# Kernel optimization log

Measured on AMD Instinct MI355X. Metric: run time of the kernel, lower is better.

## Reference

```python
import jax, jax.numpy as jnp
import numpy as np
import math


def ste_round(x):
    # round with straight-through gradient (identity in bwd)
    return x + jax.lax.stop_gradient(jnp.round(x) - x)


def ste_floor(x):
    return x + jax.lax.stop_gradient(jnp.floor(x) - x)


def _conv(x, w, b):
    # 5x5 stride-2 conv, padding=2 (kernel_size//2), NCHW/OIHW
    y = jax.lax.conv_general_dilated(
        x, w, window_strides=(2, 2), padding=[(2, 2), (2, 2)],
        dimension_numbers=('NCHW', 'OIHW', 'NCHW'))
    return y + b[None, :, None, None]


def _split_conv(x, w, b_int, mul, split=4):
    # 4 redundant sub-convolutions with floor-STE quantized integer weights/biases
    wq = ste_round(w)  # wSTE: round-to-int with STE
    out = 0.0
    for i in range(split):
        out = out + _conv(x, ste_floor((wq + i) / split), ste_floor((b_int + i) / split))
    return out * mul[None, :, None, None]


def _forward(x, w0, b0, w1, b1, w2, b2, w3, b3, mul0, mul1, mul2, mul3,
             relu0, relu1, relu2, md0, md1, md2, md3, ga_left):
    Bits = 8; clp_k = 8; in_scale = 8; scl_k = 3
    relus = [relu0, relu1, relu2]
    clp = [round((2 ** Bits - 1) / r * 2 ** (16 + clp_k)) for r in relus]
    scl = [math.floor((r + 2 ** (scl_k - 1)) / 2 ** scl_k) for r in relus]

    # quantize input to uint8 range
    x = jnp.clip(ste_round(x * 2 ** in_scale), 0, 255)

    # ---- layer 0 ----
    x = _split_conv(x, w0, ste_round(b0 * 2 ** in_scale), mul0)
    x = ste_floor((x + 2.0 ** (md0 - 1 + in_scale - clp_k)) / 2.0 ** (md0 + in_scale - clp_k))
    x = jnp.clip(x, 0, clp[0])
    x = ste_floor((ste_round(x * scl[0]) + 2.0 ** (15 + clp_k - scl_k)) / 2.0 ** (16 + clp_k - scl_k))

    # ---- layers 1, 2 ----
    for w_, b_, mul_, md_, idx in ((w1, b1, mul1, md1, 1), (w2, b2, mul2, md2, 2)):
        x = _split_conv(x, w_, ste_round(b_), mul_)
        x = ste_floor((x + 2.0 ** (md_ - 1 - clp_k)) / 2.0 ** (md_ - clp_k))
        x = jnp.clip(x, 0, clp[idx])
        x = ste_floor((ste_round(x * scl[idx]) + 2.0 ** (15 + clp_k - scl_k)) / 2.0 ** (16 + clp_k - scl_k))

    # ---- layer 3 (latent) ----
    x = _split_conv(x, w3, ste_round(b3), mul3)
    x = ste_floor((x + 2.0 ** (md3 - 1 - ga_left)) / 2.0 ** (md3 - ga_left))
    return x


def setup_inputs():
    key = jax.random.key(0)
    ks = jax.random.split(key, 16)
    N, M = 192, 320
    d = {}
    d['x'] = jax.random.uniform(ks[0], (4, 3, 512, 512), dtype=jnp.float32)
    # float weights whose round() gives small ints (integerized LIC weights)
    d['w0'] = jax.random.normal(ks[1], (N, 3, 5, 5), dtype=jnp.float32) * 3.0
    d['b0'] = jax.random.normal(ks[2], (N,), dtype=jnp.float32)
    d['w1'] = jax.random.normal(ks[3], (N, N, 5, 5), dtype=jnp.float32) * 3.0
    d['b1'] = jax.random.normal(ks[4], (N,), dtype=jnp.float32) * 16.0
    d['w2'] = jax.random.normal(ks[5], (N, N, 5, 5), dtype=jnp.float32) * 3.0
    d['b2'] = jax.random.normal(ks[6], (N,), dtype=jnp.float32) * 16.0
    d['w3'] = jax.random.normal(ks[7], (M, N, 5, 5), dtype=jnp.float32) * 3.0
    d['b3'] = jax.random.normal(ks[8], (M,), dtype=jnp.float32) * 16.0
    # per-channel integer-valued fixed-point multipliers
    d['mul0'] = jax.random.randint(ks[9], (N,), 1, 64).astype(jnp.float32)
    d['mul1'] = jax.random.randint(ks[10], (N,), 1, 64).astype(jnp.float32)
    d['mul2'] = jax.random.randint(ks[11], (N,), 1, 64).astype(jnp.float32)
    d['mul3'] = jax.random.randint(ks[12], (M,), 1, 64).astype(jnp.float32)
    d['relu0'] = 65536; d['relu1'] = 65536; d['relu2'] = 65536
    d['md0'] = 7; d['md1'] = 15; d['md2'] = 15; d['md3'] = 10
    d['ga_left'] = 4
    return d


def reference(x, w0, b0, w1, b1, w2, b2, w3, b3, mul0, mul1, mul2, mul3,
              relu0, relu1, relu2, md0, md1, md2, md3, ga_left):
    return _forward(x, w0, b0, w1, b1, w2, b2, w3, b3, mul0, mul1, mul2, mul3,
                    relu0, relu1, relu2, md0, md1, md2, md3, ga_left)
```

## Files before the change

### kernel.cpp

```cpp
#include <hip/hip_runtime.h>
#include <hip/hip_bf16.h>

typedef int i32x4 __attribute__((ext_vector_type(4)));
typedef unsigned int u32;
typedef unsigned long long u64;
typedef long long ll;

__device__ __forceinline__ void load_lds16(const void* g, void* l) {
  __builtin_amdgcn_global_load_lds(
      (const __attribute__((address_space(1))) u32*)g,
      (__attribute__((address_space(3))) u32*)l, 16, 0, 0);
}

__global__ __launch_bounds__(256) void prep_all(
    const float* __restrict__ w0, const float* __restrict__ w1,
    const float* __restrict__ w2, const float* __restrict__ w3,
    signed char* __restrict__ w0q, signed char* __restrict__ w1p,
    signed char* __restrict__ w2p, signed char* __restrict__ w3p,
    signed char* __restrict__ zbuf,
    int* __restrict__ totw0, int* __restrict__ totw1,
    int* __restrict__ totw2, int* __restrict__ totw3)
{
  __shared__ signed char ldsw[8 * 4800];
  const int blk = blockIdx.x;
  const int tid = threadIdx.x;

  if (blk < 88) {
    const float* wsrc; signed char* wdst; int* tot; int MF, sub;
    if (blk < 24)      { wsrc = w1; wdst = w1p; tot = totw1; MF = 12; sub = blk; }
    else if (blk < 48) { wsrc = w2; wdst = w2p; tot = totw2; MF = 12; sub = blk - 24; }
    else               { wsrc = w3; wdst = w3p; tot = totw3; MF = 20; sub = blk - 48; }
    const int mf = sub >> 1, half = sub & 1, colbase = half * 8;
    const int ocb = mf * 16 + colbase;
    for (int o = 0; o < 8; o++) {
      const float* src = wsrc + (size_t)(ocb + o) * 4800;
      int s = 0;
      for (int j = tid; j < 4800; j += 256) {
        int v = (int)rintf(src[j]);
        ldsw[o * 4800 + j] = (signed char)v;
        s += v;
      }
      atomicAdd(&tot[ocb + o], s);
    }
    __syncthreads();
    for (int u = tid; u < 9600; u += 256) {
      int eu = u & 3, colL = (u >> 2) & 7, q = (u >> 5) & 3, t = u >> 7;
      int tap = t / 3, ch = t - 3 * tap;
      int ci0 = ch * 64 + q * 16 + eu * 4;
      const signed char* sp = ldsw + colL * 4800 + tap;
      u32 wv = 0;
      #pragma unroll
      for (int bb = 0; bb < 4; bb++)
        wv |= ((u32)(unsigned char)sp[(ci0 + bb) * 25]) << (8 * bb);
      *(u32*)(wdst + ((size_t)t * MF + mf) * 1024 +
              (q * 16 + colbase + colL) * 16 + eu * 4) = wv;
    }
  } else {
    if (tid < 128) ((u64*)zbuf)[tid] = 0x8080808080808080ULL;
    for (int i = tid; i < 24576; i += 256) {
      int e = i & 15, colA = (i >> 4) & 15, q = (i >> 8) & 3, t = i >> 10;
      int mf = t % 12, ch = t / 12;
      signed char v = 0;
      if (e < 15 && (ch == 0 || q == 0)) {
        int ky = (ch == 0) ? q : 4;
        int ci = e / 5, kx = e - ci * 5;
        v = (signed char)(int)rintf(
            w0[((mf * 16 + colA) * 3 + ci) * 25 + ky * 5 + kx]);
      }
      w0q[i] = v;
    }
    for (int oc = tid; oc < 192; oc += 256) {
      const float* p = w0 + (size_t)oc * 75;
      int s = 0;
      #pragma unroll 5
      for (int j = 0; j < 75; j++) s += (int)rintf(p[j]);
      totw0[oc] = s;
    }
  }
}

__global__ __launch_bounds__(192, 3) void conv0F(
    const float* __restrict__ x, const signed char* __restrict__ wq,
    const float* __restrict__ bias, const float* __restrict__ mulv,
    const int* __restrict__ totw,
    const int* __restrict__ reluP, const int* __restrict__ mdP,
    unsigned char* __restrict__ outA)
{
  __shared__ signed char ilds[3][5][132];

  const int tid = threadIdx.x;
  const int lane = tid & 63;
  const int col = lane & 15;
  const int quad = lane >> 4;
  const int w = tid >> 6;
  const int blk = blockIdx.x;
  const int oxblk = blk & 3;
  const int oy = (blk >> 2) & 255;
  const int b = blk >> 10;
  const int oxbase = oxblk * 64;

  i32x4 afr[2][4];
  #pragma unroll
  for (int ch = 0; ch < 2; ch++)
    #pragma unroll
    for (int i = 0; i < 4; i++)
      afr[ch][i] = *(const i32x4*)(wq + ch * 12288 + (w * 4 + i) * 1024 + lane * 16);

  const float* xb = x + (size_t)b * 3 * 512 * 512;
  for (int i = tid; i < 990; i += 192) {
    int j = i % 66; int t = i / 66; int r = t % 5; int ci = t / 5;
    int iy = 2 * oy - 2 + r;
    int ix = 2 * oxbase - 2 + 2 * j;
    int v0 = -128, v1 = -128;
    if ((unsigned)iy < 512u) {
      const float* row = xb + ((size_t)ci * 512 + iy) * 512;
      if ((unsigned)ix < 512u) {
        float xv = rintf(row[ix] * 256.0f);
        v0 = (int)fminf(fmaxf(xv, 0.0f), 255.0f) - 128;
      }
      if ((unsigned)(ix + 1) < 512u) {
        float xv = rintf(row[ix + 1] * 256.0f);
        v1 = (int)fminf(fmaxf(xv, 0.0f), 255.0f) - 128;
      }
    }
    *(unsigned short*)&ilds[ci][r][2 * j] =
        (unsigned short)((v0 & 0xFF) | ((v1 & 0xFF) << 8));
  }
  __syncthreads();

  i32x4 acc[4][4];
  #pragma unroll
  for (int fm = 0; fm < 4; fm++)
    #pragma unroll
    for (int fn = 0; fn < 4; fn++) acc[fm][fn] = (i32x4){0, 0, 0, 0};

  #pragma unroll
  for (int ch = 0; ch < 2; ch++) {
    const int row = (ch == 0) ? quad : 4;
    i32x4 bfr[4];
    #pragma unroll
    for (int fn = 0; fn < 4; fn++) {
      const int xb2 = 2 * (fn * 16 + col);
      const int o8 = (xb2 & 3) * 8;
      const int ab = xb2 & ~3;
      u64 w0_, w1_, w2_;
      {
        const u32* p0 = (const u32*)&ilds[0][row][ab];
        const u32* p1 = (const u32*)&ilds[1][row][ab];
        const u32* p2 = (const u32*)&ilds[2][row][ab];
        w0_ = (u64)p0[0] | ((u64)p0[1] << 32);
        w1_ = (u64)p1[0] | ((u64)p1[1] << 32);
        w2_ = (u64)p2[0] | ((u64)p2[1] << 32);
      }
      u32 a0 = (u32)(w0_ >> o8);
      u32 a1 = ((u32)(w0_ >> (o8 + 32)) & 0xFFu) | (((u32)(w1_ >> o8)) << 8);
      u32 a2 = ((u32)(w1_ >> (o8 + 24)) & 0xFFFFu) | (((u32)(w2_ >> o8)) << 16);
      u32 a3 = (u32)(w2_ >> (o8 + 16));
      bfr[fn] = (i32x4){(int)a0, (int)a1, (int)a2, (int)a3};
    }
    #pragma unroll
    for (int fm = 0; fm < 4; fm++)
      #pragma unroll
      for (int fn = 0; fn < 4; fn++)
        acc[fm][fn] = __builtin_amdgcn_mfma_i32_16x16x64_i8(
            afr[ch][fm], bfr[fn], acc[fm][fn], 0, 0, 0);
  }

  const size_t pix0 = ((size_t)(b * 256 + oy)) * 256 + oxbase;
  const int rl = reluP[0];
  const int sh = mdP[0];
  const ll clpv_ll = llrint(255.0 / (double)rl * 16777216.0);
  const int clpv = clpv_ll > 0x7FFFFFFFLL ? 0x7FFFFFFF : (int)clpv_ll;
  const int sclv = (int)((rl + 4) >> 3);
  const int rnd = 1 << (sh - 1);
  #pragma unroll
  for (int fm = 0; fm < 4; fm++) {
    const int oc0 = w * 64 + fm * 16 + quad * 4;
    int bim[4], mu32[4];
    #pragma unroll
    for (int r = 0; r < 4; r++) {
      int bi = (int)llrintf(bias[oc0 + r] * 256.0f) + 128 * totw[oc0 + r];
      mu32[r] = (int)llrintf(mulv[oc0 + r]);
      bim[r] = bi * mu32[r];
    }
    #pragma unroll
    for (int fn = 0; fn < 4; fn++) {
      const size_t pix = pix0 + fn * 16 + col;
      u32 wd = 0;
      #pragma unroll
      for (int r = 0; r < 4; r++) {
        int vi = acc[fm][fn][r] * mu32[r] + bim[r];
        int y = (vi + rnd) >> sh;
        y = y < 0 ? 0 : (y > clpv ? clpv : y);
        y = (y * sclv + (1 << 20)) >> 21;
        wd |= (((u32)y ^ 0x80u) & 0xFFu) << (8 * r);
      }
      *(u32*)(outA + pix * 192 + oc0) = wd;
    }
  }
}

template <int COUT, int HIN, int WIN, int HOUT, int WOUT, int WV,
          int KSPLIT, bool DIRECT, int NH>
__global__ __launch_bounds__(WV * 64, 2) void convS(
    const signed char* __restrict__ act, const signed char* __restrict__ wp,
    const float* __restrict__ bias, const float* __restrict__ mulv,
    const int* __restrict__ totw,
    const int* __restrict__ reluP, const int* __restrict__ mdP,
    const signed char* __restrict__ zbuf,
    unsigned char* __restrict__ outA, int* __restrict__ outP)
{
  constexpr int CIN = 192;
  constexpr int PASSES = 4;
  constexpr int MF = COUT / 16;
  constexpr int OCW = COUT / WV;
  constexpr int FM = OCW / 16;
  constexpr int SAe = MF * 1024;
  constexpr int TX = WOUT / (16 * NH);
  constexpr int TYB = HOUT / 4;
  constexpr int TPP = 25 / KSPLIT;
  constexpr int NSTEP = TPP * 3;
  constexpr int NB = PASSES * NH;
  constexpr int BUFB = NB * 1024;
  constexpr int SMAX = (NB + WV - 1) / WV;
  constexpr int PSZ = 4 * HOUT * WOUT * COUT;
  static_assert(WV * OCW == COUT, "M covers COUT");
  static_assert(NSTEP >= 4, "pipeline depth");

  __shared__ __align__(16) char smem[4 * BUFB];

  const int tid = threadIdx.x;
  const int lane = tid & 63;
  const int col = lane & 15;
  const int quad = lane >> 4;
  const int w = tid >> 6;
  const int part = blockIdx.y;

  int bx = blockIdx.x;
  const int tx = bx % TX; bx /= TX;
  const int ty = bx % TYB;
  const int b = bx / TYB;
  const int ox0 = tx * 16 * NH;
  const int oy0 = ty * 4;
  const int tap0 = part * TPP;

  const signed char* bp[SMAX];
  int mjx[SMAX], mjy[SMAX];
  #pragma unroll
  for (int k = 0; k < SMAX; k++) {
    const int j = w + k * WV;
    if (j < NB) {
      const int p = j / NH, h = j % NH;
      const int oxv = ox0 + h * 16 + col;
      const int oyv = oy0 + p;
      bp[k] = act + ((size_t)b * HIN * WIN + (size_t)(2 * oyv) * WIN + 2 * oxv) * CIN
              + quad * 16;
      int mx = 0, my = 0;
      #pragma unroll
      for (int kk = 0; kk < 5; kk++) {
        if ((unsigned)(2 * oxv + kk - 2) < (unsigned)WIN) mx |= 1 << kk;
        if ((unsigned)(2 * oyv + kk - 2) < (unsigned)HIN) my |= 1 << kk;
      }
      mjx[k] = mx; mjy[k] = my;
    }
  }
  int kyS = tap0 / 5, kxS = tap0 - 5 * kyS, chS = 0;
  auto stage = [&](int sel) {
    const int offB = ((kyS - 2) * WIN + (kxS - 2)) * CIN + chS * 64;
    #pragma unroll
    for (int k = 0; k < SMAX; k++) {
      const int j = w + k * WV;
      if (j < NB) {
        bool v = ((mjx[k] >> kxS) & 1) && ((mjy[k] >> kyS) & 1);
        const signed char* g = v ? (bp[k] + offB) : (zbuf + quad * 16);
        load_lds16(g, smem + sel * BUFB + j * 1024);
      }
    }
    chS++;
    if (chS == 3) { chS = 0; kxS++; if (kxS == 5) { kxS = 0; kyS++; } }
  };

  i32x4 acc[FM][NB];
  #pragma unroll
  for (int fm = 0; fm < FM; fm++)
    #pragma unroll
    for (int j = 0; j < NB; j++) acc[fm][j] = (i32x4){0, 0, 0, 0};

  const signed char* aptr = wp + (size_t)(tap0 * 3) * SAe + w * FM * 1024 + lane * 16;
  i32x4 aA[FM], aB[FM];
  #pragma unroll
  for (int i = 0; i < FM; i++) aA[i] = *(const i32x4*)(aptr + i * 1024);

  auto comp = [&](int base, i32x4 (&a)[FM]) {
    const char* pB = smem + base + lane * 16;
    i32x4 bfr[NB];
    #pragma unroll
    for (int i = 0; i < NB; i++)
      bfr[i] = *(const i32x4*)(pB + i * 1024);
    #pragma unroll
    for (int fm = 0; fm < FM; fm++)
      #pragma unroll
      for (int j = 0; j < NB; j++)
        acc[fm][j] = __builtin_amdgcn_mfma_i32_16x16x64_i8(
            a[fm], bfr[j], acc[fm][j], 0, 0, 0);
  };

  stage(0); stage(1); stage(2);
  if constexpr (SMAX == 2) asm volatile("s_waitcnt vmcnt(4)" ::: "memory");
  else                     asm volatile("s_waitcnt vmcnt(2)" ::: "memory");
  asm volatile("s_barrier" ::: "memory");

  int sl = 0;
  #pragma unroll 1
  for (; sl + 1 < NSTEP; sl += 2) {
    aptr += SAe;
    #pragma unroll
    for (int i = 0; i < FM; i++) aB[i] = *(const i32x4*)(aptr + i * 1024);
    if (sl + 3 < NSTEP) stage((sl + 3) & 3);
    comp((sl & 3) * BUFB, aA);
    asm volatile("s_barrier" ::: "memory");
    if (sl + 2 < NSTEP) {
      aptr += SAe;
      #pragma unroll
      for (int i = 0; i < FM; i++) aA[i] = *(const i32x4*)(aptr + i * 1024);
    }
    if (sl + 4 < NSTEP) stage((sl + 4) & 3);
    comp(((sl + 1) & 3) * BUFB, aB);
    if (sl + 2 < NSTEP) asm volatile("s_barrier" ::: "memory");
  }
  if (sl < NSTEP) {
    comp((sl & 3) * BUFB, aA);
  }

  if constexpr (DIRECT) {
    const int rl = reluP[0];
    const int sh = mdP[0] - 8;
    const ll clpv = llrint(255.0 / (double)rl * 16777216.0);
    const ll sclv = (ll)((rl + 4) >> 3);
    #pragma unroll
    for (int fm = 0; fm < FM; fm++) {
      const int oc0 = w * OCW + fm * 16 + quad * 4;
      ll bi[4], mu[4];
      #pragma unroll
      for (int r = 0; r < 4; r++) {
        bi[r] = llrintf(bias[oc0 + r]) + 128LL * totw[oc0 + r];
        mu[r] = llrintf(mulv[oc0 + r]);
      }
      #pragma unroll
      for (int j = 0; j < NB; j++) {
        const int p = j / NH, h = j % NH;
        const int oyv = oy0 + p;
        const int oxv = ox0 + h * 16 + col;
        u32 wd = 0;
        #pragma unroll
        for (int r = 0; r < 4; r++) {
          ll vi = ((ll)acc[fm][j][r] + bi[r]) * mu[r];
          ll y = (vi + (1LL << (sh - 1))) >> sh;
          y = y < 0 ? 0LL : (y > clpv ? clpv : y);
          y = (y * sclv + (1LL << 20)) >> 21;
          wd |= (((u32)y ^ 0x80u) & 0xFFu) << (8 * r);
        }
        *(u32*)(outA + ((size_t)((b * HOUT + oyv) * WOUT + oxv)) * COUT + oc0) = wd;
      }
    }
  } else {
    int* pout = outP + (size_t)part * PSZ;
    #pragma unroll
    for (int fm = 0; fm < FM; fm++) {
      const int oc0 = w * OCW + fm * 16 + quad * 4;
      #pragma unroll
      for (int j = 0; j < NB; j++) {
        const int p = j / NH, h = j % NH;
        const int oyv = oy0 + p;
        const int oxv = ox0 + h * 16 + col;
        *(i32x4*)(pout + ((size_t)((b * HOUT + oyv) * WOUT + oxv)) * COUT + oc0) =
            acc[fm][j];
      }
    }
  }
}

__global__ __launch_bounds__(256) void reduce2(
    const int* __restrict__ partP, const float* __restrict__ bias,
    const float* __restrict__ mulv, const int* __restrict__ totw,
    const int* __restrict__ reluP, const int* __restrict__ mdP,
    unsigned char* __restrict__ outA)
{
  const int gid = blockIdx.x * 256 + threadIdx.x;
  const int PSZ4 = 4 * 64 * 64 * 192 / 4;
  const int4* pp = (const int4*)partP;
  int4 sv = pp[gid];
  #pragma unroll
  for (int p = 1; p < 5; p++) {
    int4 v = pp[(size_t)p * PSZ4 + gid];
    sv.x += v.x; sv.y += v.y; sv.z += v.z; sv.w += v.w;
  }
  int sa[4] = {sv.x, sv.y, sv.z, sv.w};
  const int oc0 = (gid * 4) % 192;
  const int rl = reluP[0];
  const int sh = mdP[0] - 8;
  const ll clpv = llrint(255.0 / (double)rl * 16777216.0);
  const ll sclv = (ll)((rl + 4) >> 3);
  u32 wd = 0;
  #pragma unroll
  for (int r = 0; r < 4; r++) {
    ll bi = llrintf(bias[oc0 + r]) + 128LL * totw[oc0 + r];
    ll mu = llrintf(mulv[oc0 + r]);
    ll vi = ((ll)sa[r] + bi) * mu;
    ll y = (vi + (1LL << (sh - 1))) >> sh;
    y = y < 0 ? 0LL : (y > clpv ? clpv : y);
    y = (y * sclv + (1LL << 20)) >> 21;
    wd |= (((u32)y ^ 0x80u) & 0xFFu) << (8 * r);
  }
  ((u32*)outA)[gid] = wd;
}

__global__ __launch_bounds__(256) void reduce3(
    const int* __restrict__ partP, const float* __restrict__ b3,
    const float* __restrict__ mul3, const int* __restrict__ totw3,
    const int* __restrict__ mdP, const int* __restrict__ gaP,
    float* __restrict__ outF)
{
  const int gid = blockIdx.x * 256 + threadIdx.x;
  int t = gid;
  const int ox = t & 31; t >>= 5;
  const int oy = t & 31; t >>= 5;
  const int oc = t % 320;
  const int b  = t / 320;
  const int PSZ = 4 * 32 * 32 * 320;
  const size_t src = ((size_t)((b * 32 + oy) * 32 + ox)) * 320 + oc;
  ll s = 0;
  #pragma unroll
  for (int p = 0; p < 5; p++) s += partP[(size_t)p * PSZ + src];
  const int sh = mdP[0] - gaP[0];
  const ll bi = llrintf(b3[oc]) + 128LL * totw3[oc];
  const ll mu = llrintf(mul3[oc]);
  const ll y = ((s + bi) * mu + (1LL << (sh - 1))) >> sh;
  outF[gid] = (float)y;
}

extern "C" void kernel_launch(void* const* d_in, const int* in_sizes, int n_in,
                              void* d_out, int out_size, void* d_ws, size_t ws_size,
                              hipStream_t stream)
{
  const float* x    = (const float*)d_in[0];
  const float* w0   = (const float*)d_in[1];
  const float* b0   = (const float*)d_in[2];
  const float* w1   = (const float*)d_in[3];
  const float* b1   = (const float*)d_in[4];
  const float* w2   = (const float*)d_in[5];
  const float* b2   = (const float*)d_in[6];
  const float* w3   = (const float*)d_in[7];
  const float* b3   = (const float*)d_in[8];
  const float* mul0 = (const float*)d_in[9];
  const float* mul1 = (const float*)d_in[10];
  const float* mul2 = (const float*)d_in[11];
  const float* mul3 = (const float*)d_in[12];
  const int* relu0  = (const int*)d_in[13];
  const int* relu1  = (const int*)d_in[14];
  const int* relu2  = (const int*)d_in[15];
  const int* md0    = (const int*)d_in[16];
  const int* md1    = (const int*)d_in[17];
  const int* md2    = (const int*)d_in[18];
  const int* md3    = (const int*)d_in[19];
  const int* ga     = (const int*)d_in[20];

  char* ws = (char*)d_ws;
  size_t off = 0;
  signed char* zbuf = (signed char*)(ws + off); off += 1024;
  signed char* w0q  = (signed char*)(ws + off); off += 24576;
  signed char* w1p  = (signed char*)(ws + off); off += 921600;
  signed char* w2p  = (signed char*)(ws + off); off += 921600;
  signed char* w3p  = (signed char*)(ws + off); off += 1536000;
  int*         totw1= (int*)        (ws + off); off += 192 * 4;
  int*         totw2= (int*)        (ws + off); off += 192 * 4;
  int*         totw3= (int*)        (ws + off); off += 320 * 4;
  int*         totw0= (int*)        (ws + off); off += 192 * 4;
  unsigned char* act1 = (unsigned char*)(ws + off); off += (size_t)4 * 256 * 256 * 192;
  unsigned char* act2 = (unsigned char*)(ws + off); off += (size_t)4 * 128 * 128 * 192;
  unsigned char* act3 = (unsigned char*)(ws + off); off += (size_t)4 * 64 * 64 * 192;
  int*         partl  = (int*)(ws + off); off += (size_t)5 * 4 * 64 * 64 * 192 * 4;
  (void)ws_size; (void)in_sizes; (void)n_in; (void)out_size;

  hipMemsetAsync(totw1, 0, (192 + 192 + 320 + 192) * 4, stream);
  prep_all<<<89, 256, 0, stream>>>(w0, w1, w2, w3, w0q, w1p, w2p, w3p,
                                   zbuf, totw0, totw1, totw2, totw3);
  conv0F<<<4096, 192, 0, stream>>>(x, w0q, b0, mul0, totw0, relu0, md0, act1);
  convS<192, 256, 256, 128, 128, 4, 1, true, 2><<<dim3(512, 1), 256, 0, stream>>>(
      (const signed char*)act1, w1p, b1, mul1, totw1, relu1, md1, zbuf, act2, nullptr);
  convS<192, 128, 128, 64, 64, 4, 5, false, 2><<<dim3(128, 5), 256, 0, stream>>>(
      (const signed char*)act2, w2p, b2, mul2, totw2, relu2, md2, zbuf, nullptr, partl);
  reduce2<<<3072, 256, 0, stream>>>(partl, b2, mul2, totw2, relu2, md2, act3);
  convS<320, 64, 64, 32, 32, 5, 5, false, 1><<<dim3(64, 5), 320, 0, stream>>>(
      (const signed char*)act3, w3p, b3, mul3, totw3, nullptr, md3, zbuf, nullptr, partl);
  reduce3<<<5120, 256, 0, stream>>>(partl, b3, mul3, totw3, md3, ga, (float*)d_out);
}
```

Before: 332.5 us.

## Deepen conv staging to a six-slot LDS ring with two MFMA steps per barrier

```diff
diff --git a/kernel.cpp b/kernel.cpp
--- a/kernel.cpp
+++ b/kernel.cpp
@@ -222,12 +222,15 @@
   constexpr int NSTEP = TPP * 3;
   constexpr int NB = PASSES * NH;
   constexpr int BUFB = NB * 1024;
+  constexpr int RING = 6;
   constexpr int SMAX = (NB + WV - 1) / WV;
+  constexpr int NSUP2 = NSTEP / 4;
+  constexpr int VC = 2 * (NB >= WV ? NB / WV : 1);
   constexpr int PSZ = 4 * HOUT * WOUT * COUT;
   static_assert(WV * OCW == COUT, "M covers COUT");
-  static_assert(NSTEP >= 4, "pipeline depth");
-
-  __shared__ __align__(16) char smem[4 * BUFB];
+  static_assert(NSTEP % 4 == 3, "tail structure assumes NSTEP = 4k+3");
+
+  __shared__ __align__(16) char smem[RING * BUFB];
 
   const int tid = threadIdx.x;
   const int lane = tid & 63;
@@ -265,7 +268,8 @@
     }
   }
   int kyS = tap0 / 5, kxS = tap0 - 5 * kyS, chS = 0;
-  auto stage = [&](int sel) {
+  int ssl = 0;
+  auto stage = [&]() {
     const int offB = ((kyS - 2) * WIN + (kxS - 2)) * CIN + chS * 64;
     #pragma unroll
     for (int k = 0; k < SMAX; k++) {
@@ -273,11 +277,12 @@
       if (j < NB) {
         bool v = ((mjx[k] >> kxS) & 1) && ((mjy[k] >> kyS) & 1);
         const signed char* g = v ? (bp[k] + offB) : (zbuf + quad * 16);
-        load_lds16(g, smem + sel * BUFB + j * 1024);
+        load_lds16(g, smem + ssl * BUFB + j * 1024);
       }
     }
     chS++;
     if (chS == 3) { chS = 0; kxS++; if (kxS == 5) { kxS = 0; kyS++; } }
+    ssl = (ssl + 1 == RING) ? 0 : ssl + 1;
   };
 
   i32x4 acc[FM][NB];
@@ -286,13 +291,16 @@
     #pragma unroll
     for (int j = 0; j < NB; j++) acc[fm][j] = (i32x4){0, 0, 0, 0};
 
-  const signed char* aptr = wp + (size_t)(tap0 * 3) * SAe + w * FM * 1024 + lane * 16;
-  i32x4 aA[FM], aB[FM];
-  #pragma unroll
-  for (int i = 0; i < FM; i++) aA[i] = *(const i32x4*)(aptr + i * 1024);
-
-  auto comp = [&](int base, i32x4 (&a)[FM]) {
-    const char* pB = smem + base + lane * 16;
+  auto loadA = [&](int u, i32x4 (&dst)[FM]) {
+    const signed char* p = wp + (size_t)(tap0 * 3 + u) * SAe + w * FM * 1024 + lane * 16;
+    #pragma unroll
+    for (int i = 0; i < FM; i++) dst[i] = *(const i32x4*)(p + i * 1024);
+  };
+
+  int rb = 0;
+  auto cslot = [&]() { int t = rb; rb = (rb + 1 == RING) ? 0 : rb + 1; return t; };
+  auto comp = [&](int slot, i32x4 (&a)[FM]) {
+    const char* pB = smem + slot * BUFB + lane * 16;
     i32x4 bfr[NB];
     #pragma unroll
     for (int i = 0; i < NB; i++)
@@ -305,32 +313,30 @@
             a[fm], bfr[j], acc[fm][j], 0, 0, 0);
   };
 
-  stage(0); stage(1); stage(2);
-  if constexpr (SMAX == 2) asm volatile("s_waitcnt vmcnt(4)" ::: "memory");
-  else                     asm volatile("s_waitcnt vmcnt(2)" ::: "memory");
+  i32x4 a0[FM], a1[FM], a2[FM], a3[FM];
+  loadA(0, a0); loadA(1, a1);
+  stage(); stage(); stage(); stage();
+  if constexpr (VC == 4) asm volatile("s_waitcnt vmcnt(4)" ::: "memory");
+  else                   asm volatile("s_waitcnt vmcnt(2)" ::: "memory");
   asm volatile("s_barrier" ::: "memory");
 
-  int sl = 0;
   #pragma unroll 1
-  for (; sl + 1 < NSTEP; sl += 2) {
-    aptr += SAe;
-    #pragma unroll
-    for (int i = 0; i < FM; i++) aB[i] = *(const i32x4*)(aptr + i * 1024);
-    if (sl + 3 < NSTEP) stage((sl + 3) & 3);
-    comp((sl & 3) * BUFB, aA);
+  for (int i2 = 0; i2 < NSUP2; ++i2) {
+    const int u0 = 4 * i2;
+    loadA(u0 + 2, a2); loadA(u0 + 3, a3);
+    stage(); stage();
+    comp(cslot(), a0); comp(cslot(), a1);
     asm volatile("s_barrier" ::: "memory");
-    if (sl + 2 < NSTEP) {
-      aptr += SAe;
-      #pragma unroll
-      for (int i = 0; i < FM; i++) aA[i] = *(const i32x4*)(aptr + i * 1024);
-    }
-    if (sl + 4 < NSTEP) stage((sl + 4) & 3);
-    comp(((sl + 1) & 3) * BUFB, aB);
-    if (sl + 2 < NSTEP) asm volatile("s_barrier" ::: "memory");
-  }
-  if (sl < NSTEP) {
-    comp((sl & 3) * BUFB, aA);
-  }
+    loadA(u0 + 4, a0); loadA(u0 + 5, a1);
+    stage();
+    if (u0 + 7 < NSTEP) stage();
+    comp(cslot(), a2); comp(cslot(), a3);
+    asm volatile("s_barrier" ::: "memory");
+  }
+  loadA(NSTEP - 1, a2);
+  comp(cslot(), a0); comp(cslot(), a1);
+  asm volatile("s_barrier" ::: "memory");
+  comp(cslot(), a2);
 
   if constexpr (DIRECT) {
     const int rl = reluP[0];
```

Measured after the change: 343.7 us. 1.03x slower.

## Split layers 2 and 3 convolutions by input-channel chunk instead of tap range

Applied to the files above, without the earlier changes.

```diff
diff --git a/kernel.cpp b/kernel.cpp
--- a/kernel.cpp
+++ b/kernel.cpp
@@ -112,16 +112,12 @@
     int iy = 2 * oy - 2 + r;
     int ix = 2 * oxbase - 2 + 2 * j;
     int v0 = -128, v1 = -128;
-    if ((unsigned)iy < 512u) {
-      const float* row = xb + ((size_t)ci * 512 + iy) * 512;
-      if ((unsigned)ix < 512u) {
-        float xv = rintf(row[ix] * 256.0f);
-        v0 = (int)fminf(fmaxf(xv, 0.0f), 255.0f) - 128;
-      }
-      if ((unsigned)(ix + 1) < 512u) {
-        float xv = rintf(row[ix + 1] * 256.0f);
-        v1 = (int)fminf(fmaxf(xv, 0.0f), 255.0f) - 128;
-      }
+    if ((unsigned)iy < 512u && (unsigned)ix < 512u) {
+      const float2 xv = *(const float2*)(xb + ((size_t)ci * 512 + iy) * 512 + ix);
+      float a0 = rintf(xv.x * 256.0f);
+      float a1 = rintf(xv.y * 256.0f);
+      v0 = (int)fminf(fmaxf(a0, 0.0f), 255.0f) - 128;
+      v1 = (int)fminf(fmaxf(a1, 0.0f), 255.0f) - 128;
     }
     *(unsigned short*)&ilds[ci][r][2 * j] =
         (unsigned short)((v0 & 0xFF) | ((v1 & 0xFF) << 8));
@@ -201,7 +197,7 @@
 }
 
 template <int COUT, int HIN, int WIN, int HOUT, int WOUT, int WV,
-          int KSPLIT, bool DIRECT, int NH>
+          int NPART, bool CHS, bool DIRECT, int NH>
 __global__ __launch_bounds__(WV * 64, 2) void convS(
     const signed char* __restrict__ act, const signed char* __restrict__ wp,
     const float* __restrict__ bias, const float* __restrict__ mulv,
@@ -216,10 +212,11 @@
   constexpr int OCW = COUT / WV;
   constexpr int FM = OCW / 16;
   constexpr int SAe = MF * 1024;
+  constexpr int ASTRIDE = CHS ? 3 * SAe : SAe;
   constexpr int TX = WOUT / (16 * NH);
   constexpr int TYB = HOUT / 4;
-  constexpr int TPP = 25 / KSPLIT;
-  constexpr int NSTEP = TPP * 3;
+  constexpr int TPP = CHS ? 25 : 25 / NPART;
+  constexpr int NSTEP = CHS ? 25 : TPP * 3;
   constexpr int NB = PASSES * NH;
   constexpr int BUFB = NB * 1024;
   constexpr int SMAX = (NB + WV - 1) / WV;
@@ -242,7 +239,7 @@
   const int b = bx / TYB;
   const int ox0 = tx * 16 * NH;
   const int oy0 = ty * 4;
-  const int tap0 = part * TPP;
+  const int tap0 = CHS ? 0 : part * TPP;
 
   const signed char* bp[SMAX];
   int mjx[SMAX], mjy[SMAX];
@@ -264,7 +261,8 @@
       mjx[k] = mx; mjy[k] = my;
     }
   }
-  int kyS = tap0 / 5, kxS = tap0 - 5 * kyS, chS = 0;
+  int kyS = tap0 / 5, kxS = tap0 - 5 * kyS;
+  int chS = CHS ? part : 0;
   auto stage = [&](int sel) {
     const int offB = ((kyS - 2) * WIN + (kxS - 2)) * CIN + chS * 64;
     #pragma unroll
@@ -276,8 +274,12 @@
         load_lds16(g, smem + sel * BUFB + j * 1024);
       }
     }
-    chS++;
-    if (chS == 3) { chS = 0; kxS++; if (kxS == 5) { kxS = 0; kyS++; } }
+    if constexpr (CHS) {
+      kxS++; if (kxS == 5) { kxS = 0; kyS++; }
+    } else {
+      chS++;
+      if (chS == 3) { chS = 0; kxS++; if (kxS == 5) { kxS = 0; kyS++; } }
+    }
   };
 
   i32x4 acc[FM][NB];
@@ -286,7 +288,8 @@
     #pragma unroll
     for (int j = 0; j < NB; j++) acc[fm][j] = (i32x4){0, 0, 0, 0};
 
-  const signed char* aptr = wp + (size_t)(tap0 * 3) * SAe + w * FM * 1024 + lane * 16;
+  const signed char* aptr = wp + (size_t)(CHS ? part : tap0 * 3) * SAe
+                            + w * FM * 1024 + lane * 16;
   i32x4 aA[FM], aB[FM];
   #pragma unroll
   for (int i = 0; i < FM; i++) aA[i] = *(const i32x4*)(aptr + i * 1024);
@@ -313,14 +316,14 @@
   int sl = 0;
   #pragma unroll 1
   for (; sl + 1 < NSTEP; sl += 2) {
-    aptr += SAe;
+    aptr += ASTRIDE;
     #pragma unroll
     for (int i = 0; i < FM; i++) aB[i] = *(const i32x4*)(aptr + i * 1024);
     if (sl + 3 < NSTEP) stage((sl + 3) & 3);
     comp((sl & 3) * BUFB, aA);
     asm volatile("s_barrier" ::: "memory");
     if (sl + 2 < NSTEP) {
-      aptr += SAe;
+      aptr += ASTRIDE;
       #pragma unroll
       for (int i = 0; i < FM; i++) aA[i] = *(const i32x4*)(aptr + i * 1024);
     }
@@ -391,7 +394,7 @@
   const int4* pp = (const int4*)partP;
   int4 sv = pp[gid];
   #pragma unroll
-  for (int p = 1; p < 5; p++) {
+  for (int p = 1; p < 3; p++) {
     int4 v = pp[(size_t)p * PSZ4 + gid];
     sv.x += v.x; sv.y += v.y; sv.z += v.z; sv.w += v.w;
   }
@@ -431,7 +434,7 @@
   const size_t src = ((size_t)((b * 32 + oy) * 32 + ox)) * 320 + oc;
   ll s = 0;
   #pragma unroll
-  for (int p = 0; p < 5; p++) s += partP[(size_t)p * PSZ + src];
+  for (int p = 0; p < 3; p++) s += partP[(size_t)p * PSZ + src];
   const int sh = mdP[0] - gaP[0];
   const ll bi = llrintf(b3[oc]) + 128LL * totw3[oc];
   const ll mu = llrintf(mul3[oc]);
@@ -486,12 +489,12 @@
   prep_all<<<89, 256, 0, stream>>>(w0, w1, w2, w3, w0q, w1p, w2p, w3p,
                                    zbuf, totw0, totw1, totw2, totw3);
   conv0F<<<4096, 192, 0, stream>>>(x, w0q, b0, mul0, totw0, relu0, md0, act1);
-  convS<192, 256, 256, 128, 128, 4, 1, true, 2><<<dim3(512, 1), 256, 0, stream>>>(
+  convS<192, 256, 256, 128, 128, 4, 1, false, true, 2><<<dim3(512, 1), 256, 0, stream>>>(
       (const signed char*)act1, w1p, b1, mul1, totw1, relu1, md1, zbuf, act2, nullptr);
-  convS<192, 128, 128, 64, 64, 4, 5, false, 2><<<dim3(128, 5), 256, 0, stream>>>(
+  convS<192, 128, 128, 64, 64, 4, 3, true, false, 2><<<dim3(128, 3), 256, 0, stream>>>(
       (const signed char*)act2, w2p, b2, mul2, totw2, relu2, md2, zbuf, nullptr, partl);
   reduce2<<<3072, 256, 0, stream>>>(partl, b2, mul2, totw2, relu2, md2, act3);
-  convS<320, 64, 64, 32, 32, 5, 5, false, 1><<<dim3(64, 5), 320, 0, stream>>>(
+  convS<320, 64, 64, 32, 32, 5, 3, true, false, 1><<<dim3(64, 3), 320, 0, stream>>>(
       (const signed char*)act3, w3p, b3, mul3, totw3, nullptr, md3, zbuf, nullptr, partl);
   reduce3<<<5120, 256, 0, stream>>>(partl, b3, mul3, totw3, md3, ga, (float*)d_out);
 }
```

After: 316.0 us. -5.0%, faster.
